# Kernel optimization log

Measured on AMD Instinct MI355X. Metric: run time of the kernel, lower is better.

Reference implementation:

```python
import jax, jax.numpy as jnp
import numpy as np

EMBED_DIM = 1024
NUM_HEADS = 16
HEAD_DIM = EMBED_DIM // NUM_HEADS
LN_EPS = 1e-5


def setup_inputs() -> dict:
    key = jax.random.key(0)
    ks = jax.random.split(key, 6)
    b, s, d = 2, 2048, EMBED_DIM
    scale = 1.0 / np.sqrt(d)
    x = jax.random.normal(ks[0], (b, s, d), dtype=jnp.float32)
    w_qkv = jax.random.normal(ks[1], (d, 3 * d), dtype=jnp.float32) * scale
    b_qkv = jax.random.normal(ks[2], (3 * d,), dtype=jnp.float32) * 0.02
    w_out = jax.random.normal(ks[3], (d, d), dtype=jnp.float32) * scale
    b_out = jax.random.normal(ks[4], (d,), dtype=jnp.float32) * 0.02
    gamma = jnp.ones((d,), dtype=jnp.float32)
    ln_beta = jnp.zeros((d,), dtype=jnp.float32)
    beta = jax.random.normal(ks[5], (), dtype=jnp.float32) * 0.1
    return {"x": x, "w_qkv": w_qkv, "b_qkv": b_qkv, "w_out": w_out,
            "b_out": b_out, "gamma": gamma, "ln_beta": ln_beta, "beta": beta}


def _layernorm(x, gamma, ln_beta):
    mu = jnp.mean(x, axis=-1, keepdims=True)
    var = jnp.mean(jnp.square(x - mu), axis=-1, keepdims=True)
    return (x - mu) * jax.lax.rsqrt(var + LN_EPS) * gamma + ln_beta


def reference(x, w_qkv, b_qkv, w_out, b_out, gamma, ln_beta, beta):
    b, s, d = x.shape
    h, hd = NUM_HEADS, HEAD_DIM
    residual = x
    xn = _layernorm(x, gamma, ln_beta)
    qkv = xn @ w_qkv + b_qkv                       # [b, s, 3d]
    qkv = qkv.reshape(b, s, 3, h, hd)
    q = jnp.transpose(qkv[:, :, 0], (0, 2, 1, 3))  # [b, h, s, hd]
    k = jnp.transpose(qkv[:, :, 1], (0, 2, 1, 3))
    v = jnp.transpose(qkv[:, :, 2], (0, 2, 1, 3))
    attn = jnp.einsum('bhqd,bhkd->bhqk', q, k) / np.sqrt(hd)
    idx = jnp.arange(s)
    dist = jnp.abs(idx[None, :] - idx[:, None]).astype(attn.dtype)  # [s, s]
    attn = attn + beta * jnp.log1p(dist)[None, None, :, :]
    probs = jax.nn.softmax(attn, axis=-1)
    ctx = jnp.einsum('bhqk,bhkd->bhqd', probs, v)  # [b, h, s, hd]
    ctx = jnp.transpose(ctx, (0, 2, 1, 3)).reshape(b, s, d)
    return residual + ctx @ w_out + b_out
```

## Files before the change

kernel.cpp:

```cpp
#include <hip/hip_runtime.h>

#define SEQ 2048
#define DIM 1024
#define NHEAD 16
#define HDIM 64
#define NTOK 4096
#define N3D 3072

typedef __attribute__((ext_vector_type(8))) short bf16x8;
typedef __attribute__((ext_vector_type(4))) float floatx4;
typedef __attribute__((ext_vector_type(4))) unsigned short ushortx4;

__device__ __forceinline__ unsigned short f2bf(float f) {
    unsigned int u = __builtin_bit_cast(unsigned int, f);
    u += 0x7FFFu + ((u >> 16) & 1u);
    return (unsigned short)(u >> 16);
}

__device__ __forceinline__ void async_copy16(const void* g, const void* l) {
    __builtin_amdgcn_global_load_lds(
        (const __attribute__((address_space(1))) unsigned int*)(unsigned long long)g,
        (__attribute__((address_space(3))) unsigned int*)(unsigned int)(unsigned long long)l,
        16, 0, 0);
}

#define MFMA_BF16(a, b, c) __builtin_amdgcn_mfma_f32_16x16x32_bf16((a), (b), (c), 0, 0, 0)

__global__ __launch_bounds__(256)
void prep_kernel(const float* __restrict__ w_qkv, unsigned short* __restrict__ wqkvT,
                 const float* __restrict__ w_out, unsigned short* __restrict__ woutT,
                 const float* __restrict__ x, const float* __restrict__ gamma,
                 const float* __restrict__ lnb, unsigned short* __restrict__ xn) {
    const int bid = blockIdx.x;
    const int tid = threadIdx.x;
    if (bid < 4096) {
        __shared__ float tile[32][33];
        const float* src; unsigned short* dst; int cols, bx, by;
        if (bid < 3072) { src = w_qkv; dst = wqkvT; cols = N3D; bx = bid % 96; by = bid / 96; }
        else { int t = bid - 3072; src = w_out; dst = woutT; cols = DIM; bx = t & 31; by = t >> 5; }
        const int c0 = bx * 32, r0 = by * 32;
        const int tx = tid & 31, ty = tid >> 5;
        for (int i = 0; i < 4; ++i) {
            int r = ty + i * 8;
            tile[r][tx] = src[(size_t)(r0 + r) * cols + c0 + tx];
        }
        __syncthreads();
        for (int i = 0; i < 4; ++i) {
            int rr = ty + i * 8;
            dst[(size_t)(c0 + rr) * DIM + r0 + tx] = f2bf(tile[tx][rr]);
        }
    } else {
        const int row = bid - 4096;
        const float* xr = x + (size_t)row * DIM;
        float4 v = ((const float4*)xr)[tid];
        float s = v.x + v.y + v.z + v.w;
        float s2 = v.x * v.x + v.y * v.y + v.z * v.z + v.w * v.w;
        for (int off = 1; off < 64; off <<= 1) {
            s += __shfl_xor(s, off, 64);
            s2 += __shfl_xor(s2, off, 64);
        }
        __shared__ float red[8];
        const int wave = tid >> 6, lane = tid & 63;
        if (lane == 0) { red[wave] = s; red[4 + wave] = s2; }
        __syncthreads();
        s = red[0] + red[1] + red[2] + red[3];
        s2 = red[4] + red[5] + red[6] + red[7];
        const float mu = s * (1.0f / DIM);
        const float var = s2 * (1.0f / DIM) - mu * mu;
        const float rstd = rsqrtf(var + 1e-5f);
        float4 g = ((const float4*)gamma)[tid];
        float4 bb = ((const float4*)lnb)[tid];
        unsigned short* o = xn + (size_t)row * DIM + tid * 4;
        o[0] = f2bf((v.x - mu) * rstd * g.x + bb.x);
        o[1] = f2bf((v.y - mu) * rstd * g.y + bb.y);
        o[2] = f2bf((v.z - mu) * rstd * g.z + bb.z);
        o[3] = f2bf((v.w - mu) * rstd * g.w + bb.w);
    }
}

__global__ __launch_bounds__(256)
void qkv_gemm(const unsigned short* __restrict__ A, const unsigned short* __restrict__ Bt,
              const float* __restrict__ bias, unsigned short* __restrict__ qo,
              unsigned short* __restrict__ ko, unsigned short* __restrict__ vTo) {
    __shared__ unsigned short Asm[128 * 64];
    __shared__ unsigned short Bsm[128 * 64];
    const int tid = threadIdx.x;
    const int wave = tid >> 6, lane = tid & 63;
    const int quad = lane >> 4, r16 = lane & 15;
    const int flat = blockIdx.y * 24 + blockIdx.x;
    const int swz = (flat & 7) * 96 + (flat >> 3);
    const int m0 = (swz / 24) * 128, n0 = (swz % 24) * 128;
    const int wm = (wave & 1) * 64, wn = (wave >> 1) * 64;
    floatx4 acc[4][4] = {};
    for (int k0 = 0; k0 < DIM; k0 += 64) {
        __syncthreads();
        for (int p = 0; p < 4; ++p) {
            int s = tid + p * 256;
            int r = s >> 3, c8 = (s & 7) << 3;
            async_copy16(A + (size_t)(m0 + r) * DIM + k0 + c8, Asm + s * 8);
            async_copy16(Bt + (size_t)(n0 + r) * DIM + k0 + c8, Bsm + s * 8);
        }
        __syncthreads();
        for (int h = 0; h < 2; ++h) {
            bf16x8 af[4], bfr[4];
            for (int i = 0; i < 4; ++i)
                af[i] = *(const bf16x8*)(Asm + (wm + i * 16 + r16) * 64 + h * 32 + quad * 8);
            for (int j = 0; j < 4; ++j)
                bfr[j] = *(const bf16x8*)(Bsm + (wn + j * 16 + r16) * 64 + h * 32 + quad * 8);
            for (int i = 0; i < 4; ++i)
                for (int j = 0; j < 4; ++j)
                    acc[i][j] = MFMA_BF16(af[i], bfr[j], acc[i][j]);
        }
    }
    for (int j = 0; j < 4; ++j) {
        int n = n0 + wn + j * 16 + r16;
        float bn = bias[n];
        int part = n >> 10, nn = n & 1023;
        int head = nn >> 6, hdi = nn & 63;
        for (int i = 0; i < 4; ++i) {
            int mbase = m0 + wm + i * 16 + quad * 4;
            int bIdx = mbase >> 11, sIdx = mbase & 2047;
            if (part == 2) {
                ushortx4 pack;
                for (int e = 0; e < 4; ++e) pack[e] = f2bf(acc[i][j][e] + bn);
                *(ushortx4*)(vTo + ((size_t)(bIdx * NHEAD + head) * HDIM + hdi) * SEQ + sIdx) = pack;
            } else {
                unsigned short* dst = (part == 0) ? qo : ko;
                for (int e = 0; e < 4; ++e)
                    dst[((size_t)(bIdx * NHEAD + head) * SEQ + sIdx + e) * HDIM + hdi] =
                        f2bf(acc[i][j][e] + bn);
            }
        }
    }
}

__global__ __launch_bounds__(512)
void attn_kernel(const unsigned short* __restrict__ qg, const unsigned short* __restrict__ kg,
                 const unsigned short* __restrict__ vTg, const float* __restrict__ betap,
                 unsigned short* __restrict__ ctx) {
    __shared__ unsigned short QP[128][72];
    __shared__ unsigned short Kd[2][64 * 64];
    __shared__ unsigned short Vd[2][64 * 64];
    __shared__ float logt[SEQ];

    const int tid = threadIdx.x;
    const int wave = tid >> 6, lane = tid & 63;
    const int quad = lane >> 4, r16 = lane & 15;
    const int flat = blockIdx.y * 16 + blockIdx.x;
    const int swz = (flat & 7) * 64 + (flat >> 3);
    const int bh = swz >> 4, qt = swz & 15;
    const int qBase = qt * 128;
    const float betaV = betap[0];
    const float L2E = 1.44269504f;
    const float c1 = 0.125f * L2E;

    for (int i = tid; i < SEQ; i += 512)
        logt[i] = betaV * log1pf((float)i) * L2E - 20.0f;

    const unsigned short* qptr = qg + ((size_t)bh * SEQ + qBase) * HDIM;
    for (int s = tid; s < 1024; s += 512) {
        int r = s >> 3, c8 = (s & 7) << 3;
        *(bf16x8*)(&QP[r][c8]) = *(const bf16x8*)(qptr + r * HDIM + c8);
    }

    const int sr = tid >> 3;
    const int scg = (tid & 7) ^ (sr & 7);
    const unsigned short* kbh = kg + (size_t)bh * SEQ * HDIM;
    const unsigned short* vbh = vTg + (size_t)bh * HDIM * SEQ;
    async_copy16(kbh + (size_t)sr * HDIM + scg * 8, &Kd[0][tid * 8]);
    async_copy16(vbh + (size_t)sr * SEQ + scg * 8, &Vd[0][tid * 8]);
    __syncthreads();

    bf16x8 qf0 = *(const bf16x8*)(&QP[wave * 16 + r16][quad * 8]);
    bf16x8 qf1 = *(const bf16x8*)(&QP[wave * 16 + r16][32 + quad * 8]);

    const bf16x8 onesv = {0x3F80, 0x3F80, 0x3F80, 0x3F80, 0x3F80, 0x3F80, 0x3F80, 0x3F80};

    floatx4 o[5] = {};
    const int qWaveBase = qBase + wave * 16;
    const int qrow0 = qWaveBase + quad * 4;

    for (int kt0 = 0; kt0 < SEQ; kt0 += 64) {
        const int buf = (kt0 >> 6) & 1;
        if (kt0 + 64 < SEQ) {
            async_copy16(kbh + (size_t)(kt0 + 64 + sr) * HDIM + scg * 8, &Kd[buf ^ 1][tid * 8]);
            async_copy16(vbh + (size_t)sr * SEQ + kt0 + 64 + scg * 8, &Vd[buf ^ 1][tid * 8]);
        }

        floatx4 sc[4];
        __builtin_amdgcn_s_setprio(1);
        for (int ct = 0; ct < 4; ++ct) {
            int rK = ct * 16 + r16;
            const unsigned short* kb = &Kd[buf][rK * 64];
            bf16x8 kf0 = *(const bf16x8*)(kb + ((quad ^ (rK & 7)) << 3));
            bf16x8 kf1 = *(const bf16x8*)(kb + (((quad ^ 4) ^ (rK & 7)) << 3));
            floatx4 z = {0.f, 0.f, 0.f, 0.f};
            z = MFMA_BF16(qf0, kf0, z);
            z = MFMA_BF16(qf1, kf1, z);
            sc[ct] = z;
        }
        __builtin_amdgcn_s_setprio(0);
        for (int ct = 0; ct < 4; ++ct) {
            const int keyTile = kt0 + ct * 16;
            const int key = keyTile + r16;
            if (qWaveBase >= keyTile + 16) {
                const float* lp = &logt[qrow0 - key];
                for (int i = 0; i < 4; ++i)
                    sc[ct][i] = __builtin_amdgcn_exp2f(sc[ct][i] * c1 + lp[i]);
            } else if (keyTile >= qWaveBase + 16) {
                const float* lp = &logt[key - qrow0 - 3];
                for (int i = 0; i < 4; ++i)
                    sc[ct][i] = __builtin_amdgcn_exp2f(sc[ct][i] * c1 + lp[3 - i]);
            } else {
                for (int i = 0; i < 4; ++i) {
                    int dist = qrow0 + i - key;
                    dist = dist < 0 ? -dist : dist;
                    sc[ct][i] = __builtin_amdgcn_exp2f(sc[ct][i] * c1 + logt[dist]);
                }
            }
        }
        for (int ct = 0; ct < 4; ++ct)
            for (int i = 0; i < 4; ++i)
                QP[wave * 16 + quad * 4 + i][ct * 16 + r16] = f2bf(sc[ct][i]);
        bf16x8 pf0 = *(const bf16x8*)(&QP[wave * 16 + r16][quad * 8]);
        bf16x8 pf1 = *(const bf16x8*)(&QP[wave * 16 + r16][32 + quad * 8]);
        __builtin_amdgcn_s_setprio(1);
        for (int nt = 0; nt < 4; ++nt) {
            int rV = nt * 16 + r16;
            const unsigned short* vb = &Vd[buf][rV * 64];
            bf16x8 vf0 = *(const bf16x8*)(vb + ((quad ^ (rV & 7)) << 3));
            bf16x8 vf1 = *(const bf16x8*)(vb + (((quad ^ 4) ^ (rV & 7)) << 3));
            o[nt] = MFMA_BF16(pf0, vf0, o[nt]);
            o[nt] = MFMA_BF16(pf1, vf1, o[nt]);
        }
        o[4] = MFMA_BF16(pf0, onesv, o[4]);
        o[4] = MFMA_BF16(pf1, onesv, o[4]);
        __builtin_amdgcn_s_setprio(0);

        __syncthreads();
    }

    const int b_ = bh >> 4, h_ = bh & 15;
    for (int i = 0; i < 4; ++i) {
        float inv = 1.0f / o[4][i];
        int qi = qBase + wave * 16 + quad * 4 + i;
        for (int nt = 0; nt < 4; ++nt) {
            int d = nt * 16 + r16;
            ctx[((size_t)(b_ * SEQ + qi)) * DIM + h_ * HDIM + d] = f2bf(o[nt][i] * inv);
        }
    }
}

__global__ __launch_bounds__(256)
void out_gemm(const unsigned short* __restrict__ A, const unsigned short* __restrict__ Bt,
              const float* __restrict__ bias, const float* __restrict__ resid,
              float* __restrict__ out) {
    __shared__ unsigned short Asm[128 * 64];
    __shared__ unsigned short Bsm[64 * 64];
    const int tid = threadIdx.x;
    const int wave = tid >> 6, lane = tid & 63;
    const int quad = lane >> 4, r16 = lane & 15;
    const int flat = blockIdx.y * 16 + blockIdx.x;
    const int swz = (flat & 7) * 64 + (flat >> 3);
    const int m0 = (swz >> 4) * 128, n0 = (swz & 15) * 64;
    const int wm = (wave & 1) * 64, wn = (wave >> 1) * 32;
    floatx4 acc[4][2] = {};
    for (int k0 = 0; k0 < DIM; k0 += 64) {
        __syncthreads();
        for (int p = 0; p < 4; ++p) {
            int s = tid + p * 256;
            int r = s >> 3, c8 = (s & 7) << 3;
            async_copy16(A + (size_t)(m0 + r) * DIM + k0 + c8, Asm + s * 8);
        }
        for (int p = 0; p < 2; ++p) {
            int s = tid + p * 256;
            int r = s >> 3, c8 = (s & 7) << 3;
            async_copy16(Bt + (size_t)(n0 + r) * DIM + k0 + c8, Bsm + s * 8);
        }
        __syncthreads();
        for (int h = 0; h < 2; ++h) {
            bf16x8 af[4], bfr[2];
            for (int i = 0; i < 4; ++i)
                af[i] = *(const bf16x8*)(Asm + (wm + i * 16 + r16) * 64 + h * 32 + quad * 8);
            for (int j = 0; j < 2; ++j)
                bfr[j] = *(const bf16x8*)(Bsm + (wn + j * 16 + r16) * 64 + h * 32 + quad * 8);
            for (int i = 0; i < 4; ++i)
                for (int j = 0; j < 2; ++j)
                    acc[i][j] = MFMA_BF16(af[i], bfr[j], acc[i][j]);
        }
    }
    for (int i = 0; i < 4; ++i)
        for (int j = 0; j < 2; ++j)
            for (int e = 0; e < 4; ++e) {
                int m = m0 + wm + i * 16 + quad * 4 + e;
                int n = n0 + wn + j * 16 + r16;
                out[(size_t)m * DIM + n] = acc[i][j][e] + bias[n] + resid[(size_t)m * DIM + n];
            }
}

extern "C" void kernel_launch(void* const* d_in, const int* in_sizes, int n_in,
                              void* d_out, int out_size, void* d_ws, size_t ws_size,
                              hipStream_t stream) {
    const float* x     = (const float*)d_in[0];
    const float* w_qkv = (const float*)d_in[1];
    const float* b_qkv = (const float*)d_in[2];
    const float* w_out = (const float*)d_in[3];
    const float* b_out = (const float*)d_in[4];
    const float* gamma = (const float*)d_in[5];
    const float* ln_b  = (const float*)d_in[6];
    const float* beta  = (const float*)d_in[7];
    float* out = (float*)d_out;

    char* ws = (char*)d_ws;
    const size_t MB = 1u << 20;
    unsigned short* xn    = (unsigned short*)(ws);
    unsigned short* wqkvT = (unsigned short*)(ws + 8 * MB);
    unsigned short* woutT = (unsigned short*)(ws + 14 * MB);
    unsigned short* qb    = (unsigned short*)(ws + 16 * MB);
    unsigned short* kb    = (unsigned short*)(ws + 24 * MB);
    unsigned short* vTb   = (unsigned short*)(ws + 32 * MB);
    unsigned short* ctx   = xn;

    prep_kernel<<<8192, 256, 0, stream>>>(w_qkv, wqkvT, w_out, woutT, x, gamma, ln_b, xn);
    qkv_gemm<<<dim3(24, 32), 256, 0, stream>>>(xn, wqkvT, b_qkv, qb, kb, vTb);
    attn_kernel<<<dim3(SEQ / 128, 32), 512, 0, stream>>>(qb, kb, vTb, beta, ctx);
    out_gemm<<<dim3(16, 32), 256, 0, stream>>>(ctx, woutT, b_out, x, out);
}
```

Measured before the change: 235.3 us.

## Widen QKV GEMM tiles to 128x192 and transpose attention score MFMA layout

The QKV GEMM switches from 128x128 tiles on a 24x32 grid to 128x192 tiles on a 1D grid of 512 blocks. Blocks are mapped so each XCD covers a contiguous M/N region for L2 locality, and each wave now holds a 4x6 accumulator array. In attention, the QK^T MFMA operands are swapped so each lane holds four consecutive keys of one query row. That lets probabilities be packed with v_cvt_pk_bf16_f32 into one 8-byte LDS store per tile instead of scattered 2-byte stores. The wider tile raises register and LDS use per block, which may lower occupancy.

```diff
diff --git a/kernel.cpp b/kernel.cpp
--- a/kernel.cpp
+++ b/kernel.cpp
@@ -83,36 +83,42 @@
               const float* __restrict__ bias, unsigned short* __restrict__ qo,
               unsigned short* __restrict__ ko, unsigned short* __restrict__ vTo) {
     __shared__ unsigned short Asm[128 * 64];
-    __shared__ unsigned short Bsm[128 * 64];
+    __shared__ unsigned short Bsm[192 * 64];
     const int tid = threadIdx.x;
     const int wave = tid >> 6, lane = tid & 63;
     const int quad = lane >> 4, r16 = lane & 15;
-    const int flat = blockIdx.y * 24 + blockIdx.x;
-    const int swz = (flat & 7) * 96 + (flat >> 3);
-    const int m0 = (swz / 24) * 128, n0 = (swz % 24) * 128;
-    const int wm = (wave & 1) * 64, wn = (wave >> 1) * 64;
-    floatx4 acc[4][4] = {};
+    const int flat = blockIdx.x;
+    const int xcd = flat & 7, c = flat >> 3;
+    const int mt = (xcd >> 1) * 8 + (c >> 3);
+    const int nt = (xcd & 1) * 8 + (c & 7);
+    const int m0 = mt * 128, n0 = nt * 192;
+    const int wm = (wave & 1) * 64, wn = (wave >> 1) * 96;
+    floatx4 acc[4][6] = {};
     for (int k0 = 0; k0 < DIM; k0 += 64) {
         __syncthreads();
         for (int p = 0; p < 4; ++p) {
             int s = tid + p * 256;
             int r = s >> 3, c8 = (s & 7) << 3;
             async_copy16(A + (size_t)(m0 + r) * DIM + k0 + c8, Asm + s * 8);
+        }
+        for (int p = 0; p < 6; ++p) {
+            int s = tid + p * 256;
+            int r = s >> 3, c8 = (s & 7) << 3;
             async_copy16(Bt + (size_t)(n0 + r) * DIM + k0 + c8, Bsm + s * 8);
         }
         __syncthreads();
         for (int h = 0; h < 2; ++h) {
-            bf16x8 af[4], bfr[4];
+            bf16x8 af[4], bfr[6];
             for (int i = 0; i < 4; ++i)
                 af[i] = *(const bf16x8*)(Asm + (wm + i * 16 + r16) * 64 + h * 32 + quad * 8);
-            for (int j = 0; j < 4; ++j)
+            for (int j = 0; j < 6; ++j)
                 bfr[j] = *(const bf16x8*)(Bsm + (wn + j * 16 + r16) * 64 + h * 32 + quad * 8);
             for (int i = 0; i < 4; ++i)
-                for (int j = 0; j < 4; ++j)
+                for (int j = 0; j < 6; ++j)
                     acc[i][j] = MFMA_BF16(af[i], bfr[j], acc[i][j]);
         }
     }
-    for (int j = 0; j < 4; ++j) {
+    for (int j = 0; j < 6; ++j) {
         int n = n0 + wn + j * 16 + r16;
         float bn = bias[n];
         int part = n >> 10, nn = n & 1023;
@@ -178,7 +184,7 @@
 
     floatx4 o[5] = {};
     const int qWaveBase = qBase + wave * 16;
-    const int qrow0 = qWaveBase + quad * 4;
+    const int qrT = qWaveBase + r16;
 
     for (int kt0 = 0; kt0 < SEQ; kt0 += 64) {
         const int buf = (kt0 >> 6) & 1;
@@ -195,33 +201,40 @@
             bf16x8 kf0 = *(const bf16x8*)(kb + ((quad ^ (rK & 7)) << 3));
             bf16x8 kf1 = *(const bf16x8*)(kb + (((quad ^ 4) ^ (rK & 7)) << 3));
             floatx4 z = {0.f, 0.f, 0.f, 0.f};
-            z = MFMA_BF16(qf0, kf0, z);
-            z = MFMA_BF16(qf1, kf1, z);
+            z = MFMA_BF16(kf0, qf0, z);
+            z = MFMA_BF16(kf1, qf1, z);
             sc[ct] = z;
         }
         __builtin_amdgcn_s_setprio(0);
         for (int ct = 0; ct < 4; ++ct) {
             const int keyTile = kt0 + ct * 16;
-            const int key = keyTile + r16;
+            const int kbase = keyTile + quad * 4;
             if (qWaveBase >= keyTile + 16) {
-                const float* lp = &logt[qrow0 - key];
+                const float* lp = &logt[qrT - kbase - 3];
+                for (int i = 0; i < 4; ++i)
+                    sc[ct][i] = __builtin_amdgcn_exp2f(sc[ct][i] * c1 + lp[3 - i]);
+            } else if (keyTile >= qWaveBase + 16) {
+                const float* lp = &logt[kbase - qrT];
                 for (int i = 0; i < 4; ++i)
                     sc[ct][i] = __builtin_amdgcn_exp2f(sc[ct][i] * c1 + lp[i]);
-            } else if (keyTile >= qWaveBase + 16) {
-                const float* lp = &logt[key - qrow0 - 3];
-                for (int i = 0; i < 4; ++i)
-                    sc[ct][i] = __builtin_amdgcn_exp2f(sc[ct][i] * c1 + lp[3 - i]);
             } else {
                 for (int i = 0; i < 4; ++i) {
-                    int dist = qrow0 + i - key;
+                    int dist = qrT - (kbase + i);
                     dist = dist < 0 ? -dist : dist;
                     sc[ct][i] = __builtin_amdgcn_exp2f(sc[ct][i] * c1 + logt[dist]);
                 }
             }
         }
-        for (int ct = 0; ct < 4; ++ct)
-            for (int i = 0; i < 4; ++i)
-                QP[wave * 16 + quad * 4 + i][ct * 16 + r16] = f2bf(sc[ct][i]);
+        {
+            unsigned short* prow = &QP[wave * 16 + r16][0];
+            for (int ct = 0; ct < 4; ++ct) {
+                unsigned int lo, hi;
+                asm("v_cvt_pk_bf16_f32 %0, %1, %2" : "=v"(lo) : "v"(sc[ct][0]), "v"(sc[ct][1]));
+                asm("v_cvt_pk_bf16_f32 %0, %1, %2" : "=v"(hi) : "v"(sc[ct][2]), "v"(sc[ct][3]));
+                uint2 pk; pk.x = lo; pk.y = hi;
+                *(uint2*)(prow + ct * 16 + quad * 4) = pk;
+            }
+        }
         bf16x8 pf0 = *(const bf16x8*)(&QP[wave * 16 + r16][quad * 8]);
         bf16x8 pf1 = *(const bf16x8*)(&QP[wave * 16 + r16][32 + quad * 8]);
         __builtin_amdgcn_s_setprio(1);
@@ -322,7 +335,7 @@
     unsigned short* ctx   = xn;
 
     prep_kernel<<<8192, 256, 0, stream>>>(w_qkv, wqkvT, w_out, woutT, x, gamma, ln_b, xn);
-    qkv_gemm<<<dim3(24, 32), 256, 0, stream>>>(xn, wqkvT, b_qkv, qb, kb, vTb);
+    qkv_gemm<<<512, 256, 0, stream>>>(xn, wqkvT, b_qkv, qb, kb, vTb);
     attn_kernel<<<dim3(SEQ / 128, 32), 512, 0, stream>>>(qb, kb, vTb, beta, ctx);
     out_gemm<<<dim3(16, 32), 256, 0, stream>>>(ctx, woutT, b_out, x, out);
 }
```

Result: no change. 234.1 us (-0.5%).
